# Kernel optimization log

Hardware: AMD Instinct MI355X
Metric: run time of the kernel (lower is better)

Reference implementation:

```python
import jax, jax.numpy as jnp
from jax import lax
import numpy as np

T = 8
TAU = 2.0       # LIFNode tau
VTH = 1.0       # v_threshold for IF and LIF
ALPHA = 2.0     # surrogate.ATan default alpha
BN_EPS = 1e-5

# --- ATan surrogate-gradient heaviside (spikingjelly semantics) ---
@jax.custom_vjp
def heaviside_atan(x):
    return (x >= 0.0).astype(x.dtype)

def _h_fwd(x):
    return heaviside_atan(x), x

def _h_bwd(x, g):
    sg = (ALPHA / 2.0) / (1.0 + (jnp.pi / 2.0 * ALPHA * x) ** 2)
    return (g * sg,)

heaviside_atan.defvjp(_h_fwd, _h_bwd)

# --- multi-step IF node: v += x; spike; hard reset to 0 ---
def if_node(x_seq):
    def step(v, x):
        v = v + x
        s = heaviside_atan(v - VTH)
        return (1.0 - s) * v, s
    return lax.scan(step, jnp.zeros_like(x_seq[0]), x_seq)[1]

# --- multi-step LIF node (decay_input=True, v_reset=0, hard reset) ---
def lif_node(x_seq):
    def step(v, x):
        v = v + (x - v) / TAU
        s = heaviside_atan(v - VTH)
        return (1.0 - s) * v, s
    return lax.scan(step, jnp.zeros_like(x_seq[0]), x_seq)[1]

def conv2d(x, w, b):
    y = lax.conv_general_dilated(x, w, (1, 1), 'SAME', dimension_numbers=('NCHW', 'OIHW', 'NCHW'))
    return y + b[None, :, None, None]

def bn(x, g, b, m, v):
    scale = g * lax.rsqrt(v + BN_EPS)
    return (x - m[None, :, None, None]) * scale[None, :, None, None] + b[None, :, None, None]

def maxpool2(x):
    return lax.reduce_window(x, -jnp.inf, lax.max, (1, 1, 2, 2), (1, 1, 2, 2), 'VALID')


def setup_inputs():
    key = jax.random.key(0)
    ks = jax.random.split(key, 8)
    B = 32
    f32 = jnp.float32
    d = {}
    d['x'] = jax.random.normal(ks[0], (B, 1, 48, 48), f32)
    d['conv1_w'] = jax.random.normal(ks[1], (128, 1, 3, 3), f32) * 0.2
    d['conv1_b'] = jnp.zeros((128,), f32)
    d['bn1_g'] = jnp.ones((128,), f32)
    d['bn1_b'] = jnp.zeros((128,), f32)
    d['bn1_m'] = jnp.zeros((128,), f32)
    d['bn1_v'] = jnp.ones((128,), f32)
    d['conv2_w'] = jax.random.normal(ks[2], (128, 128, 3, 3), f32) * 0.03
    d['conv2_b'] = jnp.zeros((128,), f32)
    d['bn2_g'] = jnp.ones((128,), f32)
    d['bn2_b'] = jnp.zeros((128,), f32)
    d['bn2_m'] = jnp.zeros((128,), f32)
    d['bn2_v'] = jnp.ones((128,), f32)
    d['fc1_w'] = jax.random.normal(ks[3], (1152, 128 * 12 * 12), f32) * 0.007
    d['fc1_b'] = jnp.zeros((1152,), f32)
    d['fc2_w'] = jax.random.normal(ks[4], (128, 1152), f32) * 0.03
    d['fc2_b'] = jnp.zeros((128,), f32)
    d['fc3_w'] = jax.random.normal(ks[5], (7, 128), f32) * 0.09
    d['fc3_b'] = jnp.zeros((7,), f32)
    return d


def reference(x, conv1_w, conv1_b, bn1_g, bn1_b, bn1_m, bn1_v,
              conv2_w, conv2_b, bn2_g, bn2_b, bn2_m, bn2_v,
              fc1_w, fc1_b, fc2_w, fc2_b, fc3_w, fc3_b):
    B = x.shape[0]
    # layer1 (single-step): conv + BN (eval-mode), dropout is identity at eval
    h = bn(conv2d(x, conv1_w, conv1_b), bn1_g, bn1_b, bn1_m, bn1_v)  # [B,128,48,48]
    # repeat over T timesteps
    x_step = jnp.broadcast_to(h, (T,) + h.shape)                      # [T,B,128,48,48]
    # layer2: IF -> maxpool -> conv -> BN -> IF -> maxpool
    s1 = if_node(x_step)                                              # [T,B,128,48,48]
    p1 = maxpool2(s1.reshape((T * B,) + s1.shape[2:]))                # [T*B,128,24,24]
    c2 = bn(conv2d(p1, conv2_w, conv2_b), bn2_g, bn2_b, bn2_m, bn2_v)
    s2 = if_node(c2.reshape((T, B) + c2.shape[1:]))                   # [T,B,128,24,24]
    p2 = maxpool2(s2.reshape((T * B,) + s2.shape[2:]))                # [T*B,128,12,12]
    # layer3: flatten -> fc -> LIF -> fc -> LIF -> fc -> LIF
    f = p2.reshape(T, B, -1)                                          # [T,B,18432]
    l1 = lif_node(jnp.einsum('tbi,oi->tbo', f, fc1_w) + fc1_b)        # [T,B,1152]
    l2 = lif_node(jnp.einsum('tbi,oi->tbo', l1, fc2_w) + fc2_b)       # [T,B,128]
    l3 = lif_node(jnp.einsum('tbi,oi->tbo', l2, fc3_w) + fc3_b)       # [T,B,7]
    return l3.mean(axis=0)                                            # [B,7]
```

## Files before the change

kernel.cpp:

```cpp
#include <hip/hip_runtime.h>
#include <hip/hip_bf16.h>


typedef float  f32x4  __attribute__((ext_vector_type(4)));
typedef __bf16 bf16x8 __attribute__((ext_vector_type(8)));

#define T_STEPS 8

static const size_t OFF_P1    = 0;
static const size_t OFF_PART  = 0;
static const size_t OFF_WT    = 44302336;
static const size_t OFF_P2    = 45481984;
static const size_t OFF_W2T   = 54919168;
static const size_t OFF_L1S   = 55508992;

__device__ __forceinline__ unsigned short bf16_rne(float f) {
  unsigned u = __builtin_bit_cast(unsigned, f);
  u += 0x7FFFu + ((u >> 16) & 1u);
  return (unsigned short)(u >> 16);
}
__device__ __forceinline__ float bf16_to_f(unsigned short h) {
  unsigned u = ((unsigned)h) << 16;
  return __builtin_bit_cast(float, u);
}

__device__ __forceinline__ void split_pair(float f0, float f1, unsigned& hi, unsigned& lo) {
  __hip_bfloat162 h2 = __float22bfloat162_rn(make_float2(f0, f1));
  unsigned uh; __builtin_memcpy(&uh, &h2, 4);
  float g0 = __builtin_bit_cast(float, uh << 16);
  float g1 = __builtin_bit_cast(float, uh & 0xFFFF0000u);
  __hip_bfloat162 l2 = __float22bfloat162_rn(make_float2(f0 - g0, f1 - g1));
  unsigned ul; __builtin_memcpy(&ul, &l2, 4);
  hi = uh;
  lo = ul;
}

__device__ __forceinline__ void lds_load16(const void* g, void* l) {
  auto* gp = reinterpret_cast<const __attribute__((address_space(1))) unsigned int*>(
      reinterpret_cast<uintptr_t>(g));
  auto* lp = reinterpret_cast<__attribute__((address_space(3))) unsigned int*>(
      reinterpret_cast<uintptr_t>(l));
  __builtin_amdgcn_global_load_lds(gp, lp, 16, 0, 0);
}

__global__ __launch_bounds__(256) void prep(const float* __restrict__ conv2_w,
                                            const float* __restrict__ fc2_w,
                                            short* __restrict__ wt_hi,
                                            short* __restrict__ wt_lo,
                                            float* __restrict__ w2t,
                                            uint4* __restrict__ p1pad4) {
  int i = blockIdx.x * 256 + threadIdx.x;
  if (i < 147456) {
    int tap = i >> 14;
    int oc  = (i >> 7) & 127;
    int ic  = i & 127;
    float wv = conv2_w[oc * 1152 + ic * 9 + tap];
    unsigned short h = bf16_rne(wv);
    wt_hi[i] = (short)h;
    wt_lo[i] = (short)bf16_rne(wv - bf16_to_f(h));
  } else if (i < 294912) {
    int j = i - 147456;
    int o = j & 127, k = j >> 7;
    w2t[j] = fc2_w[o * 1152 + k];
  } else if (i < 704512) {
    int k = i - 294912;
    int tb = k / 1600;
    int rem = k - tb * 1600;
    int pos = rem >> 4, c8 = rem & 15;
    int y, x;
    if (pos < 26)      { y = 0;  x = pos; }
    else if (pos < 52) { y = 25; x = pos - 26; }
    else { int jj = pos - 52; y = 1 + (jj >> 1); x = (jj & 1) * 25; }
    p1pad4[(tb * 676 + y * 26 + x) * 16 + c8] = make_uint4(0u, 0u, 0u, 0u);
  }
}

__global__ __launch_bounds__(128) void conv1_if_pool(
    const float* __restrict__ x, const float* __restrict__ w1, const float* __restrict__ b1,
    const float* __restrict__ g1, const float* __restrict__ be1, const float* __restrict__ m1,
    const float* __restrict__ vv1, short* __restrict__ p1) {
  __shared__ float patch[16];
  const int c  = threadIdx.x;
  const int sp = blockIdx.x;
  const int b  = blockIdx.y;
  const int oy = sp / 24, ox = sp % 24;
  if (c < 16) {
    int py = c >> 2, px = c & 3;
    int iy = 2 * oy - 1 + py, ix = 2 * ox - 1 + px;
    float v = 0.f;
    if (iy >= 0 && iy < 48 && ix >= 0 && ix < 48) v = x[b * 2304 + iy * 48 + ix];
    patch[c] = v;
  }
  __syncthreads();
  float w[9];
#pragma unroll
  for (int i = 0; i < 9; ++i) w[i] = w1[c * 9 + i];
  float scale = g1[c] * rsqrtf(vv1[c] + 1e-5f);
  float shift = (b1[c] - m1[c]) * scale + be1[c];
  float h[4];
#pragma unroll
  for (int p = 0; p < 4; ++p) {
    int py = p >> 1, px = p & 1;
    float s = 0.f;
#pragma unroll
    for (int dy = 0; dy < 3; ++dy)
#pragma unroll
      for (int dx = 0; dx < 3; ++dx) s += patch[(py + dy) * 4 + (px + dx)] * w[dy * 3 + dx];
    h[p] = s * scale + shift;
  }
  float va = 0.f, vb = 0.f, vc = 0.f, vd = 0.f;
  size_t base = ((size_t)b * 676 + (size_t)(1 + oy) * 26 + (1 + ox)) * 128 + c;
#pragma unroll
  for (int t = 0; t < T_STEPS; ++t) {
    va += h[0]; vb += h[1]; vc += h[2]; vd += h[3];
    bool s0 = va >= 1.f, s1 = vb >= 1.f, s2 = vc >= 1.f, s3 = vd >= 1.f;
    p1[base + (size_t)t * (32 * 676 * 128)] = (s0 | s1 | s2 | s3) ? (short)0x3F80 : (short)0;
    if (s0) va = 0.f; if (s1) vb = 0.f; if (s2) vc = 0.f; if (s3) vd = 0.f;
  }
}

__global__ __launch_bounds__(256, 2) void conv2_gemm(
    const short* __restrict__ p1pad, const short* __restrict__ wt_hi, const short* __restrict__ wt_lo,
    const float* __restrict__ conv2_b, const float* __restrict__ bn2_g, const float* __restrict__ bn2_b,
    const float* __restrict__ bn2_m, const float* __restrict__ bn2_v, short* __restrict__ p2) {
  __shared__ __align__(16) short lds[32768];
  short* ldsA  = lds;
  short* ldsBh = lds + 16384;
  short* ldsBl = lds + 24576;

  const int tid = threadIdx.x;
  const int lane = tid & 63;
  const int w = tid >> 6;
  const int wm = w & 1, wn = w >> 1;
  const int b = blockIdx.y;
  const int gy = blockIdx.x / 3;
  const int gx = blockIdx.x - gy * 3;

  const int g = (lane & 7) ^ (lane >> 3);
  int rowofsA[8], bofs[4];
#pragma unroll
  for (int j = 0; j < 8; ++j) {
    int r = w * 64 + j * 8 + (lane >> 3);
    int t = r >> 5, iy = (r >> 3) & 3, ix = r & 7;
    rowofsA[j] = (((t * 32 + b) * 676) + (4 * gy + iy) * 26 + (8 * gx + ix)) * 128 + g * 8;
  }
#pragma unroll
  for (int j = 0; j < 4; ++j) {
    int n = w * 32 + j * 8 + (lane >> 3);
    bofs[j] = n * 128 + g * 8;
  }

  f32x4 acc[8][4];
#pragma unroll
  for (int mi = 0; mi < 8; ++mi)
#pragma unroll
    for (int ni = 0; ni < 4; ++ni) acc[mi][ni] = (f32x4){0.f, 0.f, 0.f, 0.f};

#pragma unroll 1
  for (int s = 0; s < 18; ++s) {
    const int tap = s >> 1;
    const int kk = (s & 1) << 6;
    const int tapoff = ((tap / 3) * 26 + (tap % 3)) * 128;
    __syncthreads();
#pragma unroll
    for (int j = 0; j < 8; ++j) {
      lds_load16(p1pad + rowofsA[j] + tapoff + kk, ldsA + (w * 64 + j * 8) * 64 + lane * 8);
    }
    const int wtoff = tap * 16384 + kk;
#pragma unroll
    for (int j = 0; j < 4; ++j) {
      lds_load16(wt_hi + wtoff + bofs[j], ldsBh + (w * 32 + j * 8) * 64 + lane * 8);
      lds_load16(wt_lo + wtoff + bofs[j], ldsBl + (w * 32 + j * 8) * 64 + lane * 8);
    }
    __syncthreads();
#pragma unroll
    for (int ks = 0; ks < 2; ++ks) {
      const int cch = ks * 4 + (lane >> 4);
      bf16x8 a[8], bh[4], bl[4];
#pragma unroll
      for (int i = 0; i < 8; ++i) {
        int r = wm * 128 + i * 16 + (lane & 15);
        a[i] = *(const bf16x8*)(ldsA + r * 64 + ((cch ^ (r & 7)) * 8));
      }
#pragma unroll
      for (int i = 0; i < 4; ++i) {
        int n = wn * 64 + i * 16 + (lane & 15);
        bh[i] = *(const bf16x8*)(ldsBh + n * 64 + ((cch ^ (n & 7)) * 8));
        bl[i] = *(const bf16x8*)(ldsBl + n * 64 + ((cch ^ (n & 7)) * 8));
      }
#pragma unroll
      for (int mi = 0; mi < 8; ++mi)
#pragma unroll
        for (int ni = 0; ni < 4; ++ni) {
          acc[mi][ni] = __builtin_amdgcn_mfma_f32_16x16x32_bf16(a[mi], bh[ni], acc[mi][ni], 0, 0, 0);
          acc[mi][ni] = __builtin_amdgcn_mfma_f32_16x16x32_bf16(a[mi], bl[ni], acc[mi][ni], 0, 0, 0);
        }
    }
  }

  float sc[4], sh[4];
#pragma unroll
  for (int ni = 0; ni < 4; ++ni) {
    int oc = wn * 64 + ni * 16 + (lane & 15);
    sc[ni] = bn2_g[oc] * rsqrtf(bn2_v[oc] + 1e-5f);
    sh[ni] = (conv2_b[oc] - bn2_m[oc]) * sc[ni] + bn2_b[oc];
  }
  float* ybuf = (float*)lds;
  const int S = 132;
  float v[32];
#pragma unroll
  for (int q = 0; q < 32; ++q) v[q] = 0.f;
  unsigned short* p2u = (unsigned short*)p2;
  __syncthreads();
#pragma unroll
  for (int q = 0; q < 4; ++q) {
    if (wm == (q >> 1)) {
      const int mib = (q & 1) * 4;
#pragma unroll
      for (int ml = 0; ml < 4; ++ml)
#pragma unroll
        for (int ni = 0; ni < 4; ++ni)
#pragma unroll
          for (int r = 0; r < 4; ++r) {
            int lam = ml * 16 + ((lane >> 4) << 2) + r;
            int col = wn * 64 + ni * 16 + (lane & 15);
            ybuf[lam * S + col] = acc[mib + ml][ni][r] * sc[ni] + sh[ni];
          }
    }
    __syncthreads();
    if (tid < 128) {
      const int oc = tid;
#pragma unroll
      for (int tt = 0; tt < 2; ++tt) {
        int t = 2 * q + tt;
#pragma unroll
        for (int pooly = 0; pooly < 2; ++pooly) {
          unsigned short ov[4];
#pragma unroll
          for (int poolx = 0; poolx < 4; ++poolx) {
            bool any = false;
#pragma unroll
            for (int ry = 0; ry < 2; ++ry)
#pragma unroll
              for (int rx = 0; rx < 2; ++rx) {
                int iy = 2 * pooly + ry, ix = 2 * poolx + rx;
                float xx = ybuf[(tt * 32 + iy * 8 + ix) * S + oc];
                int qi = iy * 8 + ix;
                v[qi] += xx;
                bool ss = v[qi] >= 1.f;
                any |= ss;
                if (ss) v[qi] = 0.f;
              }
            ov[poolx] = any ? (unsigned short)0x3F80 : (unsigned short)0;
          }
          ushort4 o4; o4.x = ov[0]; o4.y = ov[1]; o4.z = ov[2]; o4.w = ov[3];
          *(ushort4*)(p2u + ((size_t)(t * 32 + b) * 128 + oc) * 144 + (2 * gy + pooly) * 12 + 4 * gx) = o4;
        }
      }
    }
    __syncthreads();
  }
}

__global__ __launch_bounds__(512) void fc1_gemm(const short* __restrict__ p2,
                                                const float* __restrict__ fc1_w,
                                                float* __restrict__ part) {
  __shared__ __align__(16) short lds[32768];
  short* ldsA = lds;
  short* ldsBh = lds + 16384;
  short* ldsBl = lds + 24576;

  const int tid = threadIdx.x;
  const int lane = tid & 63;
  const int w = tid >> 6;
  const int wm = w & 3, wn = w >> 2;
  const int n0 = blockIdx.x * 128;
  const int kb = blockIdx.y * 576;

  const int g = (lane & 7) ^ (lane >> 3);
  int aofs[4];
#pragma unroll
  for (int j = 0; j < 4; ++j) {
    int r = w * 32 + j * 8 + (lane >> 3);
    aofs[j] = r * 18432 + g * 8;
  }
  const int bn = tid >> 2;
  const int c0 = (tid & 3) * 2;
  const float* wrow = fc1_w + (size_t)(n0 + bn) * 18432 + c0 * 8;
  const int bpos0 = (c0 ^ (bn & 7)) * 8;
  const int bpos1 = ((c0 + 1) ^ (bn & 7)) * 8;

  f32x4 acc[4][4];
#pragma unroll
  for (int mi = 0; mi < 4; ++mi)
#pragma unroll
    for (int ni = 0; ni < 4; ++ni) acc[mi][ni] = (f32x4){0.f, 0.f, 0.f, 0.f};

  float4 q0, q1, q2, q3;
  {
    const float4* wp = (const float4*)(wrow + kb);
    q0 = wp[0]; q1 = wp[1]; q2 = wp[2]; q3 = wp[3];
  }

#pragma unroll 1
  for (int s = 0; s < 9; ++s) {
    const int koff = kb + s * 64;
    __syncthreads();
#pragma unroll
    for (int j = 0; j < 4; ++j) {
      lds_load16(p2 + aofs[j] + koff, ldsA + (w * 32 + j * 8) * 64 + lane * 8);
    }
    {
      unsigned h0, h1, h2, h3, h4, h5, h6, h7;
      unsigned l0, l1, l2, l3, l4, l5, l6, l7;
      split_pair(q0.x, q0.y, h0, l0);
      split_pair(q0.z, q0.w, h1, l1);
      split_pair(q1.x, q1.y, h2, l2);
      split_pair(q1.z, q1.w, h3, l3);
      split_pair(q2.x, q2.y, h4, l4);
      split_pair(q2.z, q2.w, h5, l5);
      split_pair(q3.x, q3.y, h6, l6);
      split_pair(q3.z, q3.w, h7, l7);
      uint4 H0; H0.x = h0; H0.y = h1; H0.z = h2; H0.w = h3;
      uint4 H1; H1.x = h4; H1.y = h5; H1.z = h6; H1.w = h7;
      uint4 L0; L0.x = l0; L0.y = l1; L0.z = l2; L0.w = l3;
      uint4 L1; L1.x = l4; L1.y = l5; L1.z = l6; L1.w = l7;
      *(uint4*)(ldsBh + bn * 64 + bpos0) = H0;
      *(uint4*)(ldsBh + bn * 64 + bpos1) = H1;
      *(uint4*)(ldsBl + bn * 64 + bpos0) = L0;
      *(uint4*)(ldsBl + bn * 64 + bpos1) = L1;
    }
    if (s < 8) {
      const float4* wp = (const float4*)(wrow + koff + 64);
      q0 = wp[0]; q1 = wp[1]; q2 = wp[2]; q3 = wp[3];
    }
    __builtin_amdgcn_sched_barrier(0);
    __syncthreads();
#pragma unroll
    for (int ks = 0; ks < 2; ++ks) {
      bf16x8 a[4], bh[4], bl[4];
      const int cch = ks * 4 + (lane >> 4);
#pragma unroll
      for (int i = 0; i < 4; ++i) {
        int r = wm * 64 + i * 16 + (lane & 15);
        a[i] = *(const bf16x8*)(ldsA + r * 64 + ((cch ^ (r & 7)) * 8));
        int n = wn * 64 + i * 16 + (lane & 15);
        bh[i] = *(const bf16x8*)(ldsBh + n * 64 + ((cch ^ (n & 7)) * 8));
        bl[i] = *(const bf16x8*)(ldsBl + n * 64 + ((cch ^ (n & 7)) * 8));
      }
#pragma unroll
      for (int mi = 0; mi < 4; ++mi)
#pragma unroll
        for (int ni = 0; ni < 4; ++ni) {
          acc[mi][ni] = __builtin_amdgcn_mfma_f32_16x16x32_bf16(a[mi], bh[ni], acc[mi][ni], 0, 0, 0);
          acc[mi][ni] = __builtin_amdgcn_mfma_f32_16x16x32_bf16(a[mi], bl[ni], acc[mi][ni], 0, 0, 0);
        }
    }
  }
  const size_t pbase = (size_t)(blockIdx.y * 9 + blockIdx.x) * 32768;
#pragma unroll
  for (int ni = 0; ni < 4; ++ni) {
    int j = wn * 64 + ni * 16 + (lane & 15);
#pragma unroll
    for (int mi = 0; mi < 4; ++mi) {
#pragma unroll
      for (int r = 0; r < 4; ++r) {
        int m = wm * 64 + mi * 16 + ((lane >> 4) << 2) + r;
        part[pbase + (size_t)m * 128 + j] = acc[mi][ni][r];
      }
    }
  }
}

__global__ __launch_bounds__(128) void fc1_reduce_lif(const float* __restrict__ part,
                                                      const float* __restrict__ fc1_b,
                                                      float* __restrict__ l1s) {
  int i = blockIdx.x * 128 + threadIdx.x;
  int b = i / 1152, n = i - b * 1152;
  int nt = n >> 7, j = n & 127;
  float bias = fc1_b[n];
  float v = 0.f;
#pragma unroll
  for (int t = 0; t < T_STEPS; ++t) {
    int m = t * 32 + b;
    float s = bias;
#pragma unroll 8
    for (int ks = 0; ks < 32; ++ks) s += part[(((size_t)ks * 9 + nt) * 256 + m) * 128 + j];
    v += (s - v) * 0.5f;
    bool sp = v >= 1.f;
    l1s[(size_t)m * 1152 + n] = sp ? 1.f : 0.f;
    if (sp) v = 0.f;
  }
}

__global__ __launch_bounds__(512) void tail(const float* __restrict__ l1s,
                                            const float* __restrict__ w2t,
                                            const float* __restrict__ b2,
                                            const float* __restrict__ w3,
                                            const float* __restrict__ b3,
                                            float* __restrict__ out) {
  __shared__ float sx[8][1152];
  __shared__ float part2[4][8][128];
  __shared__ float s2[8][128];
  __shared__ float y3[7][8];
  const int b = blockIdx.x;
  const int tid = threadIdx.x;
  for (int i = tid; i < 9216; i += 512) {
    int t = i / 1152, k = i - t * 1152;
    sx[t][k] = l1s[(size_t)(t * 32 + b) * 1152 + k];
  }
  __syncthreads();
  const int o = tid & 127, h = tid >> 7;
  float p[8];
#pragma unroll
  for (int t = 0; t < 8; ++t) p[t] = 0.f;
#pragma unroll 4
  for (int kk = 0; kk < 288; ++kk) {
    int k = h * 288 + kk;
    float wv = w2t[k * 128 + o];
#pragma unroll
    for (int t = 0; t < 8; ++t) p[t] += sx[t][k] * wv;
  }
#pragma unroll
  for (int t = 0; t < 8; ++t) part2[h][t][o] = p[t];
  __syncthreads();
  if (tid < 128) {
    float v = 0.f;
#pragma unroll
    for (int t = 0; t < 8; ++t) {
      float xx = part2[0][t][o] + part2[1][t][o] + part2[2][t][o] + part2[3][t][o] + b2[o];
      v += (xx - v) * 0.5f;
      bool s = v >= 1.f;
      s2[t][o] = s ? 1.f : 0.f;
      if (s) v = 0.f;
    }
  }
  __syncthreads();
  if (tid < 56) {
    int oo = tid >> 3, t = tid & 7;
    float d = 0.f;
    for (int k = 0; k < 128; ++k) d += s2[t][k] * w3[oo * 128 + k];
    y3[oo][t] = d + b3[oo];
  }
  __syncthreads();
  if (tid < 7) {
    float v = 0.f, a = 0.f;
#pragma unroll
    for (int t = 0; t < 8; ++t) {
      float xx = y3[tid][t];
      v += (xx - v) * 0.5f;
      bool s = v >= 1.f;
      a += s ? 1.f : 0.f;
      if (s) v = 0.f;
    }
    out[b * 7 + tid] = a * 0.125f;
  }
}

extern "C" void kernel_launch(void* const* d_in, const int* in_sizes, int n_in,
                              void* d_out, int out_size, void* d_ws, size_t ws_size,
                              hipStream_t stream) {
  const float* x       = (const float*)d_in[0];
  const float* conv1_w = (const float*)d_in[1];
  const float* conv1_b = (const float*)d_in[2];
  const float* bn1_g   = (const float*)d_in[3];
  const float* bn1_b   = (const float*)d_in[4];
  const float* bn1_m   = (const float*)d_in[5];
  const float* bn1_v   = (const float*)d_in[6];
  const float* conv2_w = (const float*)d_in[7];
  const float* conv2_b = (const float*)d_in[8];
  const float* bn2_g   = (const float*)d_in[9];
  const float* bn2_b   = (const float*)d_in[10];
  const float* bn2_m   = (const float*)d_in[11];
  const float* bn2_v   = (const float*)d_in[12];
  const float* fc1_w   = (const float*)d_in[13];
  const float* fc1_b   = (const float*)d_in[14];
  const float* fc2_w   = (const float*)d_in[15];
  const float* fc2_b   = (const float*)d_in[16];
  const float* fc3_w   = (const float*)d_in[17];
  const float* fc3_b   = (const float*)d_in[18];

  char* ws = (char*)d_ws;
  short* p1pad = (short*)(ws + OFF_P1);
  float* part  = (float*)(ws + OFF_PART);
  short* wt_hi = (short*)(ws + OFF_WT);
  short* wt_lo = wt_hi + 147456;
  short* p2    = (short*)(ws + OFF_P2);
  float* w2t   = (float*)(ws + OFF_W2T);
  float* l1s   = (float*)(ws + OFF_L1S);
  float* out   = (float*)d_out;

  prep<<<2752, 256, 0, stream>>>(conv2_w, fc2_w, wt_hi, wt_lo, w2t, (uint4*)p1pad);
  conv1_if_pool<<<dim3(576, 32), 128, 0, stream>>>(x, conv1_w, conv1_b, bn1_g, bn1_b, bn1_m, bn1_v, p1pad);
  conv2_gemm<<<dim3(18, 32), 256, 0, stream>>>(p1pad, wt_hi, wt_lo, conv2_b, bn2_g, bn2_b, bn2_m, bn2_v, p2);
  fc1_gemm<<<dim3(9, 32), 512, 0, stream>>>(p2, fc1_w, part);
  fc1_reduce_lif<<<288, 128, 0, stream>>>(part, fc1_b, l1s);
  tail<<<32, 512, 0, stream>>>(l1s, w2t, fc2_b, fc3_w, fc3_b, out);
}
```

Baseline: 355.6 us.

## Load conv2 A operand directly from global and double-buffer B tiles in LDS

The conv2 implicit-GEMM now reads the spike-input (A) fragments straight from global memory into registers instead of staging them through LDS. The weight (B) tiles go into two alternating LDS buffers, so the next step's weights load while the current step's MFMAs run. This cuts one barrier per iteration and the LDS traffic for A. In exchange, each wave re-reads A rows from global/L2 with less coalescing, and A load latency is exposed before the MFMAs.

```diff
diff --git a/kernel.cpp b/kernel.cpp
--- a/kernel.cpp
+++ b/kernel.cpp
@@ -124,9 +124,6 @@
     const float* __restrict__ conv2_b, const float* __restrict__ bn2_g, const float* __restrict__ bn2_b,
     const float* __restrict__ bn2_m, const float* __restrict__ bn2_v, short* __restrict__ p2) {
   __shared__ __align__(16) short lds[32768];
-  short* ldsA  = lds;
-  short* ldsBh = lds + 16384;
-  short* ldsBl = lds + 24576;
 
   const int tid = threadIdx.x;
   const int lane = tid & 63;
@@ -137,65 +134,94 @@
   const int gx = blockIdx.x - gy * 3;
 
   const int g = (lane & 7) ^ (lane >> 3);
-  int rowofsA[8], bofs[4];
-#pragma unroll
-  for (int j = 0; j < 8; ++j) {
-    int r = w * 64 + j * 8 + (lane >> 3);
-    int t = r >> 5, iy = (r >> 3) & 3, ix = r & 7;
-    rowofsA[j] = (((t * 32 + b) * 676) + (4 * gy + iy) * 26 + (8 * gx + ix)) * 128 + g * 8;
-  }
+  int bofs[4];
 #pragma unroll
   for (int j = 0; j < 4; ++j) {
     int n = w * 32 + j * 8 + (lane >> 3);
     bofs[j] = n * 128 + g * 8;
   }
 
+  int rowA[8];
+#pragma unroll
+  for (int i = 0; i < 8; ++i) {
+    int r = wm * 128 + i * 16 + (lane & 15);
+    int t = r >> 5, iy = (r >> 3) & 3, ix = r & 7;
+    rowA[i] = (((t * 32 + b) * 676) + (4 * gy + iy) * 26 + (8 * gx + ix)) * 128 + (lane >> 4) * 8;
+  }
+
+  auto stageB = [&](int s) {
+    const int tap = s >> 1;
+    const int kk = (s & 1) << 6;
+    const int wtoff = tap * 16384 + kk;
+    short* dst = lds + ((s & 1) << 14);
+#pragma unroll
+    for (int j = 0; j < 4; ++j) {
+      lds_load16(wt_hi + wtoff + bofs[j], dst + (w * 32 + j * 8) * 64 + lane * 8);
+      lds_load16(wt_lo + wtoff + bofs[j], dst + 8192 + (w * 32 + j * 8) * 64 + lane * 8);
+    }
+  };
+
   f32x4 acc[8][4];
 #pragma unroll
   for (int mi = 0; mi < 8; ++mi)
 #pragma unroll
     for (int ni = 0; ni < 4; ++ni) acc[mi][ni] = (f32x4){0.f, 0.f, 0.f, 0.f};
+
+  stageB(0);
+  __syncthreads();
 
 #pragma unroll 1
   for (int s = 0; s < 18; ++s) {
     const int tap = s >> 1;
     const int kk = (s & 1) << 6;
-    const int tapoff = ((tap / 3) * 26 + (tap % 3)) * 128;
-    __syncthreads();
-#pragma unroll
-    for (int j = 0; j < 8; ++j) {
-      lds_load16(p1pad + rowofsA[j] + tapoff + kk, ldsA + (w * 64 + j * 8) * 64 + lane * 8);
-    }
-    const int wtoff = tap * 16384 + kk;
-#pragma unroll
-    for (int j = 0; j < 4; ++j) {
-      lds_load16(wt_hi + wtoff + bofs[j], ldsBh + (w * 32 + j * 8) * 64 + lane * 8);
-      lds_load16(wt_lo + wtoff + bofs[j], ldsBl + (w * 32 + j * 8) * 64 + lane * 8);
-    }
-    __syncthreads();
-#pragma unroll
-    for (int ks = 0; ks < 2; ++ks) {
-      const int cch = ks * 4 + (lane >> 4);
-      bf16x8 a[8], bh[4], bl[4];
-#pragma unroll
-      for (int i = 0; i < 8; ++i) {
-        int r = wm * 128 + i * 16 + (lane & 15);
-        a[i] = *(const bf16x8*)(ldsA + r * 64 + ((cch ^ (r & 7)) * 8));
-      }
+    const int coff = ((tap / 3) * 26 + (tap % 3)) * 128 + kk;
+    const short* bufB = lds + ((s & 1) << 14);
+
+    bf16x8 a[8];
+#pragma unroll
+    for (int i = 0; i < 8; ++i)
+      a[i] = *(const bf16x8*)(p1pad + rowA[i] + coff);
+    __builtin_amdgcn_sched_barrier(0);
+    if (s < 17) stageB(s + 1);
+
+    bf16x8 bh[4], bl[4];
+    {
+      const int cch = lane >> 4;
 #pragma unroll
       for (int i = 0; i < 4; ++i) {
         int n = wn * 64 + i * 16 + (lane & 15);
-        bh[i] = *(const bf16x8*)(ldsBh + n * 64 + ((cch ^ (n & 7)) * 8));
-        bl[i] = *(const bf16x8*)(ldsBl + n * 64 + ((cch ^ (n & 7)) * 8));
-      }
-#pragma unroll
-      for (int mi = 0; mi < 8; ++mi)
-#pragma unroll
-        for (int ni = 0; ni < 4; ++ni) {
-          acc[mi][ni] = __builtin_amdgcn_mfma_f32_16x16x32_bf16(a[mi], bh[ni], acc[mi][ni], 0, 0, 0);
-          acc[mi][ni] = __builtin_amdgcn_mfma_f32_16x16x32_bf16(a[mi], bl[ni], acc[mi][ni], 0, 0, 0);
-        }
-    }
+        bh[i] = *(const bf16x8*)(bufB + n * 64 + ((cch ^ (n & 7)) * 8));
+        bl[i] = *(const bf16x8*)(bufB + 8192 + n * 64 + ((cch ^ (n & 7)) * 8));
+      }
+    }
+#pragma unroll
+    for (int mi = 0; mi < 8; ++mi)
+#pragma unroll
+      for (int ni = 0; ni < 4; ++ni) {
+        acc[mi][ni] = __builtin_amdgcn_mfma_f32_16x16x32_bf16(a[mi], bh[ni], acc[mi][ni], 0, 0, 0);
+        acc[mi][ni] = __builtin_amdgcn_mfma_f32_16x16x32_bf16(a[mi], bl[ni], acc[mi][ni], 0, 0, 0);
+      }
+
+#pragma unroll
+    for (int i = 0; i < 8; ++i)
+      a[i] = *(const bf16x8*)(p1pad + rowA[i] + coff + 32);
+    {
+      const int cch = 4 + (lane >> 4);
+#pragma unroll
+      for (int i = 0; i < 4; ++i) {
+        int n = wn * 64 + i * 16 + (lane & 15);
+        bh[i] = *(const bf16x8*)(bufB + n * 64 + ((cch ^ (n & 7)) * 8));
+        bl[i] = *(const bf16x8*)(bufB + 8192 + n * 64 + ((cch ^ (n & 7)) * 8));
+      }
+    }
+#pragma unroll
+    for (int mi = 0; mi < 8; ++mi)
+#pragma unroll
+      for (int ni = 0; ni < 4; ++ni) {
+        acc[mi][ni] = __builtin_amdgcn_mfma_f32_16x16x32_bf16(a[mi], bh[ni], acc[mi][ni], 0, 0, 0);
+        acc[mi][ni] = __builtin_amdgcn_mfma_f32_16x16x32_bf16(a[mi], bl[ni], acc[mi][ni], 0, 0, 0);
+      }
+    __syncthreads();
   }
 
   float sc[4], sh[4];
```

After: 396.2 us. +11.4%, slower.
